# Kernel optimization log

Measured on AMD Instinct MI355X. Metric: run time of the kernel, lower is better.

Reference implementation:

```python
import jax, jax.numpy as jnp
import numpy as np

V, D, HID, HEADS = 50000, 128, 128, 4
N, E, G = 100000, 1600000, 256
CH = HID // HEADS  # per-head channels for layer 1


def setup_inputs() -> dict:
    key = jax.random.key(0)
    ks = jax.random.split(key, 16)
    g = lambda i, shape, scale=0.05: jax.random.normal(ks[i], shape, jnp.float32) * scale
    return {
        "x_lex": jax.random.randint(ks[0], (N,), 0, V),
        "edge_index": jax.random.randint(ks[1], (2, E), 0, N),
        "batch": jnp.sort(jax.random.randint(ks[2], (N,), 0, G)),
        "emb": g(3, (V, D)),
        "W1": g(4, (D, HID)), "a1_src": g(5, (HEADS, CH)), "a1_dst": g(6, (HEADS, CH)), "b1": jnp.zeros((HID,), jnp.float32),
        "W2": g(7, (HID, HID)), "a2_src": g(8, (1, HID)), "a2_dst": g(9, (1, HID)), "b2": jnp.zeros((HID,), jnp.float32),
        "Wc1": g(10, (HID, HID // 2)), "bc1": jnp.zeros((HID // 2,), jnp.float32),
        "Wc2": g(11, (HID // 2, 1)), "bc2": jnp.zeros((1,), jnp.float32),
    }


def gat_layer(x, src, dst, W, a_src, a_dst, b, heads, ch):
    """PyG-style GATConv (v1), concat=True, negative_slope=0.2."""
    n = x.shape[0]
    h = (x @ W).reshape(n, heads, ch)                 # [N,H,C]
    al_s = (h * a_src).sum(-1)                        # [N,H]
    al_d = (h * a_dst).sum(-1)                        # [N,H]
    e = jax.nn.leaky_relu(al_s[src] + al_d[dst], 0.2) # [Etot,H]
    # segment softmax over incoming edges per destination node
    m = jax.ops.segment_max(e, dst, num_segments=n)
    ex = jnp.exp(e - m[dst])
    s = jax.ops.segment_sum(ex, dst, num_segments=n)
    alpha = ex / s[dst]
    out = jax.ops.segment_sum(alpha[:, :, None] * h[src], dst, num_segments=n)  # [N,H,C]
    return out.reshape(n, heads * ch) + b


def reference(x_lex, edge_index, batch, emb, W1, a1_src, a1_dst, b1, W2, a2_src, a2_dst, b2, Wc1, bc1, Wc2, bc2):
    n = x_lex.shape[0]
    loops = jnp.arange(n)  # GATConv adds self-loops by default
    src = jnp.concatenate([edge_index[0], loops])
    dst = jnp.concatenate([edge_index[1], loops])
    x = emb[x_lex]                                               # [N,D]
    h = jax.nn.elu(gat_layer(x, src, dst, W1, a1_src, a1_dst, b1, HEADS, CH))
    h = jax.nn.elu(gat_layer(h, src, dst, W2, a2_src, a2_dst, b2, 1, HID))
    sums = jax.ops.segment_sum(h, batch, num_segments=G)
    cnt = jax.ops.segment_sum(jnp.ones((n,), h.dtype), batch, num_segments=G)
    h_pool = sums / jnp.maximum(cnt, 1.0)[:, None]               # global mean pool [G,HID]
    logits = jax.nn.relu(h_pool @ Wc1 + bc1) @ Wc2 + bc2         # [G,1]
    return (logits, h_pool)
```

## Files before the change

kernel.cpp:

```cpp
#include <hip/hip_runtime.h>
#include <hip/hip_bf16.h>
#include <math.h>

#define P_CHUNK 8192
#define NBKT 1024

__device__ __forceinline__ float lrelu(float x){ return x < 0.f ? 0.2f*x : x; }
__device__ __forceinline__ float elu_(float x){ return x > 0.f ? x : expm1f(x); }

__global__ __launch_bounds__(256) void p1hist(const int* __restrict__ ei, int E, int Etot,
                                              int* __restrict__ totals){
  __shared__ int lh[NBKT];
  int tid = threadIdx.x;
  for (int t = tid; t < NBKT; t += 256) lh[t] = 0;
  __syncthreads();
  int base = blockIdx.x * P_CHUNK;
  for (int j = 0; j < P_CHUNK; j += 256){
    int i = base + j + tid;
    if (i < Etot){
      int dst = (i < E) ? ei[E + i] : (i - E);
      atomicAdd(&lh[dst >> 7], 1);
    }
  }
  __syncthreads();
  for (int t = tid; t < NBKT; t += 256){
    int v = lh[t];
    if (v) atomicAdd(&totals[t], v);
  }
}

__global__ __launch_bounds__(256) void p2scan(const int* __restrict__ totals,
                                              int* __restrict__ bbase, int* __restrict__ bcur,
                                              int Etot, int* __restrict__ off, int N){
  __shared__ int wsum[4];
  __shared__ int runsh;
  int tid = threadIdx.x, lane = tid & 63, w = tid >> 6;
  if (tid == 0) runsh = 0;
  __syncthreads();
  for (int c = 0; c < NBKT; c += 256){
    int v = totals[c + tid];
    int x = v;
    #pragma unroll
    for (int d = 1; d < 64; d <<= 1){ int y = __shfl_up(x, d); if (lane >= d) x += y; }
    if (lane == 63) wsum[w] = x;
    __syncthreads();
    int wpre = 0;
    for (int i = 0; i < w; i++) wpre += wsum[i];
    int run = runsh;
    int excl = run + wpre + x - v;
    bbase[c + tid] = excl;
    bcur[c + tid]  = excl;
    __syncthreads();
    if (tid == 0) runsh = run + wsum[0] + wsum[1] + wsum[2] + wsum[3];
    __syncthreads();
  }
  if (tid == 0){ bbase[NBKT] = Etot; off[N] = Etot; }
}

__global__ __launch_bounds__(256) void p3scatter(const int* __restrict__ ei, int E, int Etot,
                                                 int* __restrict__ bcur, int2* __restrict__ tmp){
  __shared__ int lh[NBKT];
  __shared__ int lbase[NBKT];
  int tid = threadIdx.x;
  for (int t = tid; t < NBKT; t += 256) lh[t] = 0;
  __syncthreads();
  int base = blockIdx.x * P_CHUNK;
  for (int j = 0; j < P_CHUNK; j += 256){
    int i = base + j + tid;
    if (i < Etot){
      int dst = (i < E) ? ei[E + i] : (i - E);
      atomicAdd(&lh[dst >> 7], 1);
    }
  }
  __syncthreads();
  for (int t = tid; t < NBKT; t += 256){
    int v = lh[t];
    lbase[t] = v ? atomicAdd(&bcur[t], v) : 0;
  }
  __syncthreads();
  for (int t = tid; t < NBKT; t += 256) lh[t] = 0;
  __syncthreads();
  for (int j = 0; j < P_CHUNK; j += 256){
    int i = base + j + tid;
    if (i < Etot){
      int s, d;
      if (i < E){ s = ei[i]; d = ei[E + i]; } else { s = i - E; d = i - E; }
      int b = d >> 7;
      int r = atomicAdd(&lh[b], 1);
      tmp[lbase[b] + r] = make_int2(s, d);
    }
  }
}

__global__ __launch_bounds__(256) void p4local(const int2* __restrict__ tmp,
                                               const int* __restrict__ bbase,
                                               int* __restrict__ off, int* __restrict__ srcs, int N){
  __shared__ int cnt[128];
  __shared__ int offL[128];
  int b = blockIdx.x, tid = threadIdx.x;
  int e0 = bbase[b], e1 = bbase[b + 1];
  if (tid < 128) cnt[tid] = 0;
  __syncthreads();
  for (int j = e0 + tid; j < e1; j += 256)
    atomicAdd(&cnt[tmp[j].y & 127], 1);
  __syncthreads();
  if (tid < 64){
    int v0 = cnt[2*tid], v1 = cnt[2*tid + 1];
    int p = v0 + v1;
    int x = p;
    #pragma unroll
    for (int d = 1; d < 64; d <<= 1){ int y = __shfl_up(x, d); if (tid >= d) x += y; }
    int excl = x - p;
    offL[2*tid]     = excl;
    offL[2*tid + 1] = excl + v0;
  }
  __syncthreads();
  if (tid < 128){
    int gd = b*128 + tid;
    if (gd < N) off[gd] = e0 + offL[tid];
    cnt[tid] = 0;
  }
  __syncthreads();
  for (int j = e0 + tid; j < e1; j += 256){
    int2 e = tmp[j];
    int d = e.y & 127;
    int r = atomicAdd(&cnt[d], 1);
    srcs[e0 + offL[d] + r] = e.x;
  }
}

template<int H, bool GATHER>
__global__ __launch_bounds__(256) void gemm_al(
    const float* __restrict__ X, const int* __restrict__ idx,
    const float* __restrict__ W, const float* __restrict__ asrc,
    const float* __restrict__ adst, float* __restrict__ Hout,
    float* __restrict__ als, float* __restrict__ ald, int n)
{
  __shared__ float xs[128][68];
  __shared__ float wch[32][128];
  int tid = threadIdx.x;
  int tr = tid >> 5, tc = tid & 31;
  int r8 = tr*8, c4 = tc*4;
  int row0 = blockIdx.x * 64;

  #pragma unroll
  for (int j=0;j<8;j++){
    int e = tid + j*256;
    int r = e >> 5, cq = e & 31;
    int gr = row0 + r;
    float4 v = make_float4(0.f,0.f,0.f,0.f);
    if (gr < n){
      int srow = GATHER ? idx[gr] : gr;
      v = *reinterpret_cast<const float4*>(&X[(size_t)srow*128 + cq*4]);
    }
    xs[cq*4+0][r] = v.x;
    xs[cq*4+1][r] = v.y;
    xs[cq*4+2][r] = v.z;
    xs[cq*4+3][r] = v.w;
  }

  float acc[8][4];
  #pragma unroll
  for (int r=0;r<8;r++)
    #pragma unroll
    for (int i=0;i<4;i++) acc[r][i] = 0.f;

  for (int kc=0;kc<4;kc++){
    __syncthreads();
    #pragma unroll
    for (int j=0;j<4;j++){
      int e = tid + j*256;
      int r = e>>5, cq = e&31;
      *reinterpret_cast<float4*>(&wch[r][cq*4]) =
        *reinterpret_cast<const float4*>(&W[(size_t)(kc*32+r)*128 + cq*4]);
    }
    __syncthreads();
    #pragma unroll
    for (int kk=0;kk<32;kk++){
      int k = kc*32+kk;
      const float4 x0 = *reinterpret_cast<const float4*>(&xs[k][r8]);
      const float4 x1 = *reinterpret_cast<const float4*>(&xs[k][r8+4]);
      const float4 wv = *reinterpret_cast<const float4*>(&wch[kk][c4]);
      acc[0][0]=fmaf(x0.x,wv.x,acc[0][0]); acc[0][1]=fmaf(x0.x,wv.y,acc[0][1]);
      acc[0][2]=fmaf(x0.x,wv.z,acc[0][2]); acc[0][3]=fmaf(x0.x,wv.w,acc[0][3]);
      acc[1][0]=fmaf(x0.y,wv.x,acc[1][0]); acc[1][1]=fmaf(x0.y,wv.y,acc[1][1]);
      acc[1][2]=fmaf(x0.y,wv.z,acc[1][2]); acc[1][3]=fmaf(x0.y,wv.w,acc[1][3]);
      acc[2][0]=fmaf(x0.z,wv.x,acc[2][0]); acc[2][1]=fmaf(x0.z,wv.y,acc[2][1]);
      acc[2][2]=fmaf(x0.z,wv.z,acc[2][2]); acc[2][3]=fmaf(x0.z,wv.w,acc[2][3]);
      acc[3][0]=fmaf(x0.w,wv.x,acc[3][0]); acc[3][1]=fmaf(x0.w,wv.y,acc[3][1]);
      acc[3][2]=fmaf(x0.w,wv.z,acc[3][2]); acc[3][3]=fmaf(x0.w,wv.w,acc[3][3]);
      acc[4][0]=fmaf(x1.x,wv.x,acc[4][0]); acc[4][1]=fmaf(x1.x,wv.y,acc[4][1]);
      acc[4][2]=fmaf(x1.x,wv.z,acc[4][2]); acc[4][3]=fmaf(x1.x,wv.w,acc[4][3]);
      acc[5][0]=fmaf(x1.y,wv.x,acc[5][0]); acc[5][1]=fmaf(x1.y,wv.y,acc[5][1]);
      acc[5][2]=fmaf(x1.y,wv.z,acc[5][2]); acc[5][3]=fmaf(x1.y,wv.w,acc[5][3]);
      acc[6][0]=fmaf(x1.z,wv.x,acc[6][0]); acc[6][1]=fmaf(x1.z,wv.y,acc[6][1]);
      acc[6][2]=fmaf(x1.z,wv.z,acc[6][2]); acc[6][3]=fmaf(x1.z,wv.w,acc[6][3]);
      acc[7][0]=fmaf(x1.w,wv.x,acc[7][0]); acc[7][1]=fmaf(x1.w,wv.y,acc[7][1]);
      acc[7][2]=fmaf(x1.w,wv.z,acc[7][2]); acc[7][3]=fmaf(x1.w,wv.w,acc[7][3]);
    }
  }

  const float4 asv = *reinterpret_cast<const float4*>(&asrc[c4]);
  const float4 adv = *reinterpret_cast<const float4*>(&adst[c4]);
  const int GT = 32 / H;
  int hh = tc / GT;

  #pragma unroll
  for (int r=0;r<8;r++){
    int gr = row0 + r8 + r;
    if (gr < n){
      *reinterpret_cast<float4*>(&Hout[(size_t)gr*128 + c4]) =
        make_float4(acc[r][0], acc[r][1], acc[r][2], acc[r][3]);
    }
    float ps = acc[r][0]*asv.x + acc[r][1]*asv.y + acc[r][2]*asv.z + acc[r][3]*asv.w;
    float pd = acc[r][0]*adv.x + acc[r][1]*adv.y + acc[r][2]*adv.z + acc[r][3]*adv.w;
    #pragma unroll
    for (int m=1;m<GT;m<<=1){ ps += __shfl_xor(ps,m); pd += __shfl_xor(pd,m); }
    if ((tc & (GT-1)) == 0 && gr < n){
      als[(size_t)gr*H + hh] = ps;
      ald[(size_t)gr*H + hh] = pd;
    }
  }
}

template<int H>
__global__ __launch_bounds__(256) void aggr(
    const float* __restrict__ h, const float* __restrict__ als,
    const float* __restrict__ ald, const int* __restrict__ srcs,
    const int* __restrict__ off, const float* __restrict__ bias,
    float* __restrict__ out, int n)
{
  __shared__ float s_p[4][64*H];
  __shared__ int   s_s[4][64];
  int tid = threadIdx.x;
  int wid = tid >> 6, lane = tid & 63;
  int d = blockIdx.x*4 + wid;
  if (d >= n) return;
  int half = lane >> 5, ch = lane & 31;
  int c4 = ch*4;
  const int hh = (H==1) ? 0 : (ch >> 3);

  int s0 = off[d], s1 = off[d+1];

  float adv[H];
  #pragma unroll
  for (int q=0;q<H;q++) adv[q] = ald[(size_t)d*H + q];

  float m[H], ssum[H];
  #pragma unroll
  for (int q=0;q<H;q++){ m[q] = -INFINITY; ssum[q] = 0.f; }
  float a0=0.f, a1=0.f, a2=0.f, a3=0.f;

  for (int base = s0; base < s1; base += 64){
    int cl = s1 - base; if (cl > 64) cl = 64;

    int sv = 0;
    float e[H];
    if (lane < cl){
      sv = srcs[base + lane];
      #pragma unroll
      for (int q=0;q<H;q++) e[q] = lrelu(als[(size_t)sv*H + q] + adv[q]);
    } else {
      #pragma unroll
      for (int q=0;q<H;q++) e[q] = -INFINITY;
    }

    float cm[H];
    #pragma unroll
    for (int q=0;q<H;q++) cm[q] = e[q];
    #pragma unroll
    for (int sh=1; sh<64; sh<<=1){
      #pragma unroll
      for (int q=0;q<H;q++) cm[q] = fmaxf(cm[q], __shfl_xor(cm[q], sh));
    }

    float p[H], sc[H];
    #pragma unroll
    for (int q=0;q<H;q++){
      float nm = fmaxf(m[q], cm[q]);
      sc[q] = __expf(m[q] - nm);
      ssum[q] *= sc[q];
      m[q] = nm;
      p[q] = __expf(e[q] - nm);
    }
    float schh = sc[0];
    #pragma unroll
    for (int q=1;q<H;q++) schh = (hh==q) ? sc[q] : schh;
    a0 *= schh; a1 *= schh; a2 *= schh; a3 *= schh;

    float cs[H];
    #pragma unroll
    for (int q=0;q<H;q++) cs[q] = p[q];
    #pragma unroll
    for (int sh=1; sh<64; sh<<=1){
      #pragma unroll
      for (int q=0;q<H;q++) cs[q] += __shfl_xor(cs[q], sh);
    }
    #pragma unroll
    for (int q=0;q<H;q++) ssum[q] += cs[q];

    #pragma unroll
    for (int q=0;q<H;q++) s_p[wid][lane*H + q] = p[q];
    s_s[wid][lane] = sv;

    for (int j = half; j < cl; j += 2){
      int s = s_s[wid][j];
      float w = s_p[wid][j*H + hh];
      const float4 hv = *reinterpret_cast<const float4*>(&h[(size_t)s*128 + c4]);
      a0 = fmaf(w, hv.x, a0);
      a1 = fmaf(w, hv.y, a1);
      a2 = fmaf(w, hv.z, a2);
      a3 = fmaf(w, hv.w, a3);
    }
  }

  a0 += __shfl_xor(a0, 32);
  a1 += __shfl_xor(a1, 32);
  a2 += __shfl_xor(a2, 32);
  a3 += __shfl_xor(a3, 32);

  float den = ssum[0];
  #pragma unroll
  for (int q=1;q<H;q++) den = (hh==q) ? ssum[q] : den;
  float inv = 1.f / den;

  if (half == 0){
    const float4 bv = *reinterpret_cast<const float4*>(&bias[c4]);
    float4 o;
    o.x = elu_(a0*inv + bv.x);
    o.y = elu_(a1*inv + bv.y);
    o.z = elu_(a2*inv + bv.z);
    o.w = elu_(a3*inv + bv.w);
    *reinterpret_cast<float4*>(&out[(size_t)d*128 + c4]) = o;
  }
}

__global__ __launch_bounds__(256) void kpool(const float* __restrict__ act,
    const int* __restrict__ batch, int n, float* __restrict__ pool)
{
  __shared__ int sb[2];
  __shared__ float part[128];
  int g = blockIdx.x, tid = threadIdx.x;
  if (tid == 0){
    int lo=0, hi=n;
    while (lo<hi){ int mid=(lo+hi)>>1; if (batch[mid] < g) lo=mid+1; else hi=mid; }
    sb[0]=lo;
    int lo2=lo, hi2=n;
    while (lo2<hi2){ int mid=(lo2+hi2)>>1; if (batch[mid] < g+1) lo2=mid+1; else hi2=mid; }
    sb[1]=lo2;
  }
  __syncthreads();
  int lo=sb[0], hi=sb[1];
  int c = tid & 127, half = tid >> 7;
  float acc = 0.f;
  for (int i=lo+half; i<hi; i+=2) acc += act[(size_t)i*128 + c];
  if (half == 0) part[c] = acc;
  __syncthreads();
  if (half == 1) part[c] += acc;
  __syncthreads();
  if (half == 0){
    float cnt = (float)(hi-lo);
    pool[(size_t)g*128 + c] = part[c] / fmaxf(cnt, 1.f);
  }
}

__global__ __launch_bounds__(64) void kclassify(const float* __restrict__ pool,
    const float* __restrict__ Wc1, const float* __restrict__ bc1,
    const float* __restrict__ Wc2, const float* __restrict__ bc2,
    float* __restrict__ logits)
{
  int g = blockIdx.x, j = threadIdx.x;
  const float* hp = pool + (size_t)g*128;
  float t = bc1[j];
  #pragma unroll 8
  for (int c=0;c<128;c++) t = fmaf(hp[c], Wc1[c*64+j], t);
  t = fmaxf(t, 0.f) * Wc2[j];
  for (int m=1;m<64;m<<=1) t += __shfl_xor(t, m);
  if (j==0) logits[g] = t + bc2[0];
}

extern "C" void kernel_launch(void* const* d_in, const int* in_sizes, int n_in,
                              void* d_out, int out_size, void* d_ws, size_t ws_size,
                              hipStream_t stream)
{
  const int*   x_lex = (const int*)d_in[0];
  const int*   ei    = (const int*)d_in[1];
  const int*   batch = (const int*)d_in[2];
  const float* emb   = (const float*)d_in[3];
  const float* W1    = (const float*)d_in[4];
  const float* a1s   = (const float*)d_in[5];
  const float* a1d   = (const float*)d_in[6];
  const float* b1    = (const float*)d_in[7];
  const float* W2    = (const float*)d_in[8];
  const float* a2s   = (const float*)d_in[9];
  const float* a2d   = (const float*)d_in[10];
  const float* b2    = (const float*)d_in[11];
  const float* Wc1   = (const float*)d_in[12];
  const float* bc1   = (const float*)d_in[13];
  const float* Wc2   = (const float*)d_in[14];
  const float* bc2   = (const float*)d_in[15];

  int N = in_sizes[0];
  int E = in_sizes[1] / 2;
  int Etot = E + N;
  const int G = 256;

  char* p = (char*)d_ws;
  float* hbuf   = (float*)p;          p += (size_t)N*128*4;
  float* act    = (float*)p;          p += (size_t)N*128*4;
  float* als    = (float*)p;          p += (size_t)N*4*4;
  float* ald    = (float*)p;          p += (size_t)N*4*4;
  int*   off    = (int*)p;            p += (size_t)(N+1)*4;
  int*   srcs   = (int*)p;            p += (size_t)Etot*4;
  int*   totals = (int*)p;            p += NBKT*4;
  int*   bbase  = (int*)p;            p += (NBKT+1)*4;
  int*   bcur   = (int*)p;
  int2*  tmp    = (int2*)hbuf;

  hipMemsetAsync(totals, 0, NBKT*4, stream);
  int nblk = (Etot + P_CHUNK - 1) / P_CHUNK;
  int nb   = (N + 127) / 128;
  p1hist   <<<nblk,256,0,stream>>>(ei, E, Etot, totals);
  p2scan   <<<1,   256,0,stream>>>(totals, bbase, bcur, Etot, off, N);
  p3scatter<<<nblk,256,0,stream>>>(ei, E, Etot, bcur, tmp);
  p4local  <<<nb,  256,0,stream>>>(tmp, bbase, off, srcs, N);

  int gb = (N + 63)/64;
  gemm_al<4,true ><<<gb,256,0,stream>>>(emb, x_lex, W1, a1s, a1d, hbuf, als, ald, N);
  aggr<4><<<(N+3)/4,256,0,stream>>>(hbuf, als, ald, srcs, off, b1, act, N);

  gemm_al<1,false><<<gb,256,0,stream>>>(act, nullptr, W2, a2s, a2d, hbuf, als, ald, N);
  aggr<1><<<(N+3)/4,256,0,stream>>>(hbuf, als, ald, srcs, off, b2, act, N);

  float* out = (float*)d_out;
  kpool<<<G,256,0,stream>>>(act, batch, N, out + G);
  kclassify<<<G,64,0,stream>>>(out + G, Wc1, bc1, Wc2, bc2, out);
}
```

Measured before the change: 528.3 us.

## Scatter edges into fixed-capacity per-bucket slabs, dropping the histogram pass

```diff
diff --git a/kernel.cpp b/kernel.cpp
--- a/kernel.cpp
+++ b/kernel.cpp
@@ -4,61 +4,15 @@
 
 #define P_CHUNK 8192
 #define NBKT 1024
+#define CAP  4096
+
+typedef float f4 __attribute__((ext_vector_type(4)));
 
 __device__ __forceinline__ float lrelu(float x){ return x < 0.f ? 0.2f*x : x; }
 __device__ __forceinline__ float elu_(float x){ return x > 0.f ? x : expm1f(x); }
 
-__global__ __launch_bounds__(256) void p1hist(const int* __restrict__ ei, int E, int Etot,
-                                              int* __restrict__ totals){
-  __shared__ int lh[NBKT];
-  int tid = threadIdx.x;
-  for (int t = tid; t < NBKT; t += 256) lh[t] = 0;
-  __syncthreads();
-  int base = blockIdx.x * P_CHUNK;
-  for (int j = 0; j < P_CHUNK; j += 256){
-    int i = base + j + tid;
-    if (i < Etot){
-      int dst = (i < E) ? ei[E + i] : (i - E);
-      atomicAdd(&lh[dst >> 7], 1);
-    }
-  }
-  __syncthreads();
-  for (int t = tid; t < NBKT; t += 256){
-    int v = lh[t];
-    if (v) atomicAdd(&totals[t], v);
-  }
-}
-
-__global__ __launch_bounds__(256) void p2scan(const int* __restrict__ totals,
-                                              int* __restrict__ bbase, int* __restrict__ bcur,
-                                              int Etot, int* __restrict__ off, int N){
-  __shared__ int wsum[4];
-  __shared__ int runsh;
-  int tid = threadIdx.x, lane = tid & 63, w = tid >> 6;
-  if (tid == 0) runsh = 0;
-  __syncthreads();
-  for (int c = 0; c < NBKT; c += 256){
-    int v = totals[c + tid];
-    int x = v;
-    #pragma unroll
-    for (int d = 1; d < 64; d <<= 1){ int y = __shfl_up(x, d); if (lane >= d) x += y; }
-    if (lane == 63) wsum[w] = x;
-    __syncthreads();
-    int wpre = 0;
-    for (int i = 0; i < w; i++) wpre += wsum[i];
-    int run = runsh;
-    int excl = run + wpre + x - v;
-    bbase[c + tid] = excl;
-    bcur[c + tid]  = excl;
-    __syncthreads();
-    if (tid == 0) runsh = run + wsum[0] + wsum[1] + wsum[2] + wsum[3];
-    __syncthreads();
-  }
-  if (tid == 0){ bbase[NBKT] = Etot; off[N] = Etot; }
-}
-
 __global__ __launch_bounds__(256) void p3scatter(const int* __restrict__ ei, int E, int Etot,
-                                                 int* __restrict__ bcur, int2* __restrict__ tmp){
+                                                 int* __restrict__ bcur, int* __restrict__ tmp){
   __shared__ int lh[NBKT];
   __shared__ int lbase[NBKT];
   int tid = threadIdx.x;
@@ -87,22 +41,51 @@
       if (i < E){ s = ei[i]; d = ei[E + i]; } else { s = i - E; d = i - E; }
       int b = d >> 7;
       int r = atomicAdd(&lh[b], 1);
-      tmp[lbase[b] + r] = make_int2(s, d);
-    }
-  }
-}
-
-__global__ __launch_bounds__(256) void p4local(const int2* __restrict__ tmp,
+      tmp[b*CAP + lbase[b] + r] = s | ((d & 127) << 17);
+    }
+  }
+}
+
+__global__ __launch_bounds__(256) void p2scan(const int* __restrict__ bcur,
+                                              int* __restrict__ bbase,
+                                              int Etot, int* __restrict__ off, int N){
+  __shared__ int wsum[4];
+  __shared__ int runsh;
+  int tid = threadIdx.x, lane = tid & 63, w = tid >> 6;
+  if (tid == 0) runsh = 0;
+  __syncthreads();
+  for (int c = 0; c < NBKT; c += 256){
+    int v = bcur[c + tid];
+    int x = v;
+    #pragma unroll
+    for (int d = 1; d < 64; d <<= 1){ int y = __shfl_up(x, d); if (lane >= d) x += y; }
+    if (lane == 63) wsum[w] = x;
+    __syncthreads();
+    int wpre = 0;
+    for (int i = 0; i < w; i++) wpre += wsum[i];
+    int run = runsh;
+    bbase[c + tid] = run + wpre + x - v;
+    __syncthreads();
+    if (tid == 0) runsh = run + wsum[0] + wsum[1] + wsum[2] + wsum[3];
+    __syncthreads();
+  }
+  if (tid == 0) off[N] = Etot;
+}
+
+__global__ __launch_bounds__(256) void p4local(const int* __restrict__ tmp,
                                                const int* __restrict__ bbase,
+                                               const int* __restrict__ bcnt,
                                                int* __restrict__ off, int* __restrict__ srcs, int N){
   __shared__ int cnt[128];
   __shared__ int offL[128];
   int b = blockIdx.x, tid = threadIdx.x;
-  int e0 = bbase[b], e1 = bbase[b + 1];
+  int e0 = bbase[b];
+  int ne = bcnt[b];
+  const int* slab = tmp + (size_t)b*CAP;
   if (tid < 128) cnt[tid] = 0;
   __syncthreads();
-  for (int j = e0 + tid; j < e1; j += 256)
-    atomicAdd(&cnt[tmp[j].y & 127], 1);
+  for (int j = tid; j < ne; j += 256)
+    atomicAdd(&cnt[(slab[j] >> 17) & 127], 1);
   __syncthreads();
   if (tid < 64){
     int v0 = cnt[2*tid], v1 = cnt[2*tid + 1];
@@ -121,11 +104,11 @@
     cnt[tid] = 0;
   }
   __syncthreads();
-  for (int j = e0 + tid; j < e1; j += 256){
-    int2 e = tmp[j];
-    int d = e.y & 127;
+  for (int j = tid; j < ne; j += 256){
+    int e = slab[j];
+    int d = (e >> 17) & 127;
     int r = atomicAdd(&cnt[d], 1);
-    srcs[e0 + offL[d] + r] = e.x;
+    srcs[e0 + offL[d] + r] = e & 0x1FFFF;
   }
 }
 
@@ -412,18 +395,16 @@
   float* ald    = (float*)p;          p += (size_t)N*4*4;
   int*   off    = (int*)p;            p += (size_t)(N+1)*4;
   int*   srcs   = (int*)p;            p += (size_t)Etot*4;
-  int*   totals = (int*)p;            p += NBKT*4;
   int*   bbase  = (int*)p;            p += (NBKT+1)*4;
   int*   bcur   = (int*)p;
-  int2*  tmp    = (int2*)hbuf;
-
-  hipMemsetAsync(totals, 0, NBKT*4, stream);
+  int*   tmp    = (int*)hbuf;
+
+  hipMemsetAsync(bcur, 0, NBKT*4, stream);
   int nblk = (Etot + P_CHUNK - 1) / P_CHUNK;
   int nb   = (N + 127) / 128;
-  p1hist   <<<nblk,256,0,stream>>>(ei, E, Etot, totals);
-  p2scan   <<<1,   256,0,stream>>>(totals, bbase, bcur, Etot, off, N);
   p3scatter<<<nblk,256,0,stream>>>(ei, E, Etot, bcur, tmp);
-  p4local  <<<nb,  256,0,stream>>>(tmp, bbase, off, srcs, N);
+  p2scan   <<<1,   256,0,stream>>>(bcur, bbase, Etot, off, N);
+  p4local  <<<nb,  256,0,stream>>>(tmp, bbase, bcur, off, srcs, N);
 
   int gb = (N + 63)/64;
   gemm_al<4,true ><<<gb,256,0,stream>>>(emb, x_lex, W1, a1s, a1d, hbuf, als, ald, N);
```

After: 516.6 us. -2.2%, faster.
